# Kernel tuning notes

Hardware: AMD Instinct MI355X
Metric: run time of the kernel (lower is better)

Reference implementation:

```python
import jax, jax.numpy as jnp
import numpy as np

KSIZE = 16  # sliding window length (module ksize)


def setup_inputs() -> dict:
    key = jax.random.key(0)
    k0, k1, k2, k3, k4 = jax.random.split(key, 5)
    B, L, D, H = 16, 1024, 256, 256
    s = 1.0 / np.sqrt(H)  # torch RNN default init: U(-1/sqrt(H), 1/sqrt(H))
    x = jax.random.normal(k0, (B, L, D), dtype=jnp.float32)
    W_ih = jax.random.uniform(k1, (3 * H, D), jnp.float32, -s, s)  # [r|z|n] rows
    W_hh = jax.random.uniform(k2, (3 * H, H), jnp.float32, -s, s)
    b_ih = jax.random.uniform(k3, (3 * H,), jnp.float32, -s, s)
    b_hh = jax.random.uniform(k4, (3 * H,), jnp.float32, -s, s)
    return {"x": x, "W_ih": W_ih, "W_hh": W_hh, "b_ih": b_ih, "b_hh": b_hh}


def reference(x, W_ih, W_hh, b_ih, b_hh):
    # LocalRNN forward: for each position l, run a GRU over the window
    # x[l-K+1 : l+1] (zero left-padded) and emit the final hidden state.
    # Instead of materializing the [B, L, K, D] windowed copy (torch get_K),
    # we scan over the K window steps, slicing the padded input each step.
    B, L, D = x.shape
    H = W_hh.shape[1]
    K = KSIZE
    xpad = jnp.concatenate([jnp.zeros((B, K - 1, D), x.dtype), x], axis=1)  # [B, L+K-1, D]

    def step(h, t):
        xt = jax.lax.dynamic_slice_in_dim(xpad, t, L, axis=1)  # [B, L, D] = window step t for every position
        gi = jnp.einsum('bld,gd->blg', xt, W_ih) + b_ih          # [B, L, 3H]
        gh = jnp.einsum('blh,gh->blg', h, W_hh) + b_hh           # [B, L, 3H]
        i_r, i_z, i_n = jnp.split(gi, 3, axis=-1)
        h_r, h_z, h_n = jnp.split(gh, 3, axis=-1)
        r = jax.nn.sigmoid(i_r + h_r)
        z = jax.nn.sigmoid(i_z + h_z)
        n = jnp.tanh(i_n + r * h_n)
        h_new = (1.0 - z) * n + z * h  # torch GRU update
        return h_new, None

    h0 = jnp.zeros((B, L, H), x.dtype)
    h_final, _ = jax.lax.scan(step, h0, jnp.arange(K))
    return h_final  # [B, L, H] == h.view(batch, l, output_dim)
```

## Files before the change

### kernel.cpp

```cpp
#include <hip/hip_runtime.h>
#include <hip/hip_bf16.h>
#include <cstdint>


#define B_  16
#define L_  1024
#define D_  256
#define H_  256
#define K_  16
#define MT  32
#define NROW 47
#define HS  264
#define GRS 258
#define GNS 264
#define L2E 1.44269504f

typedef __attribute__((ext_vector_type(8))) short  bf16x8;
typedef __attribute__((ext_vector_type(4))) float  floatx4;
typedef unsigned short ush;

#if __has_builtin(__builtin_amdgcn_exp2f)
#define fexp2(x) __builtin_amdgcn_exp2f(x)
#else
#define fexp2(x) exp2f(x)
#endif

__device__ __forceinline__ float bf2f(ush u) {
    union { unsigned int i; float f; } v; v.i = ((unsigned int)u) << 16; return v.f;
}
__device__ __forceinline__ ush f2bf(float f) {
    union { float f; unsigned int i; } v; v.f = f;
    unsigned int x = v.i;
    return (ush)((x + 0x7FFFu + ((x >> 16) & 1u)) >> 16);
}
__device__ __forceinline__ unsigned int pk2(float a, float b) {
    union { __hip_bfloat162 v; unsigned int u; } c;
    c.v = __float22bfloat162_rn(make_float2(a, b));
    return c.u;
}
__device__ __forceinline__ float rcpf(float x) { return __builtin_amdgcn_rcpf(x); }

#define NWR 196608
__global__ __launch_bounds__(256) void wprep(const float* __restrict__ Wih,
                                             const float* __restrict__ Whh,
                                             ush* __restrict__ Wir,
                                             ush* __restrict__ Wr) {
    int idx = blockIdx.x * 256 + threadIdx.x;
    const float* src = (idx < NWR) ? Whh : Wih;
    ush* dst         = (idx < NWR) ? Wr  : Wir;
    int e = (idx < NWR) ? idx : idx - NWR;
    int w    = e / 24576, r1 = e % 24576;
    int n    = r1 / 4096,  r2 = r1 % 4096;
    int ks   = r2 / 512,   r3 = r2 % 512;
    int lane = r3 >> 3,    j  = r3 & 7;
    int l16 = lane & 15, quad = lane >> 4;
    int gate = n >> 1, sloc = n & 1;
    int srow = gate * 256 + (2 * w + sloc) * 16 + l16;
    int scol = ks * 32 + quad * 8 + j;
    float scl = (gate < 2) ? -L2E : 2.f * L2E;
    dst[e] = f2bf(src[srow * 256 + scol] * scl);
}

__global__ __launch_bounds__(512, 2) void rnn_fused(const float* __restrict__ x,
                                                    const ush* __restrict__ Wir,
                                                    const ush* __restrict__ Wr,
                                                    const float* __restrict__ bih,
                                                    const float* __restrict__ bhh,
                                                    float* __restrict__ out) {
    __shared__ __align__(16) ush xs[48 * HS];
    __shared__ unsigned int grz[NROW * GRS];
    __shared__ __align__(16) ush gn[NROW * GNS];
    __shared__ __align__(16) ush hl[2][MT * HS];

    int tid  = threadIdx.x;
    int wave = tid >> 6, lane = tid & 63;
    int l16  = lane & 15, quad = lane >> 4, quad4 = quad * 4;
    int p0   = blockIdx.x * MT;
    int bb   = p0 >> 10, lb = p0 & 1023;
    int base = wave * 32 + l16;

    {
        const float4* x4 = (const float4*)x;
        for (int idx = tid; idx < 48 * 64; idx += 512) {
            int j = idx >> 6, c = idx & 63;
            int tok = lb - 15 + j;
            float4 v = make_float4(0.f, 0.f, 0.f, 0.f);
            if (tok >= 0 && tok < L_) v = x4[(size_t)((bb << 10) + tok) * 64 + c];
            *(uint2*)(xs + j * HS + c * 4) = make_uint2(pk2(v.x, v.y), pk2(v.z, v.w));
        }
        for (int idx = tid; idx < MT * HS / 2; idx += 512)
            ((unsigned int*)(&hl[0][0]))[idx] = 0u;
    }
    __syncthreads();

    {
        floatx4 gacc[3][6];
#pragma unroll
        for (int sl = 0; sl < 2; sl++) {
            int cs = base + sl * 16;
            float ir = -L2E * (bih[cs] + bhh[cs]);
            float iz = -L2E * (bih[256 + cs] + bhh[256 + cs]);
            float in_ = 2.f * L2E * bih[512 + cs];
#pragma unroll
            for (int mt = 0; mt < 3; mt++) {
                gacc[mt][0 + sl] = (floatx4){ir, ir, ir, ir};
                gacc[mt][2 + sl] = (floatx4){iz, iz, iz, iz};
                gacc[mt][4 + sl] = (floatx4){in_, in_, in_, in_};
            }
        }
        const ush* wp = Wir + (size_t)wave * 24576 + lane * 8;
#pragma unroll
        for (int ks = 0; ks < 8; ks++) {
            bf16x8 bw[6];
#pragma unroll
            for (int n = 0; n < 6; n++)
                bw[n] = *(const bf16x8*)(wp + ((n * 8 + ks) << 9));
#pragma unroll
            for (int mt = 0; mt < 3; mt++) {
                bf16x8 af = *(const bf16x8*)(xs + (mt * 16 + l16) * HS + ks * 32 + quad * 8);
#pragma unroll
                for (int n = 0; n < 6; n++)
                    gacc[mt][n] = __builtin_amdgcn_mfma_f32_16x16x32_bf16(
                        af, bw[n], gacc[mt][n], 0, 0, 0);
            }
        }
#pragma unroll
        for (int mt = 0; mt < 3; mt++)
#pragma unroll
            for (int sl = 0; sl < 2; sl++) {
                int cs = base + sl * 16;
#pragma unroll
                for (int r = 0; r < 4; r++) {
                    int j = mt * 16 + quad4 + r;
                    if (j < NROW) {
                        grz[j * GRS + cs] = pk2(gacc[mt][0 + sl][r], gacc[mt][2 + sl][r]);
                        gn[j * GNS + cs]  = f2bf(gacc[mt][4 + sl][r]);
                    }
                }
            }
    }

    bf16x8 wf[6][8];
    {
        const ush* wp = Wr + (size_t)wave * 24576 + lane * 8;
#pragma unroll
        for (int n = 0; n < 6; n++)
#pragma unroll
            for (int ks = 0; ks < 8; ks++)
                wf[n][ks] = *(const bf16x8*)(wp + ((n * 8 + ks) << 9));
    }
    float bn0 = 2.f * L2E * bhh[512 + base];
    float bn1 = 2.f * L2E * bhh[512 + base + 16];
    float hreg[16];
#pragma unroll
    for (int q = 0; q < 16; q++) hreg[q] = 0.f;
    __syncthreads();

    for (int t = 0; t < K_; t++) {
        const ush* hc  = &hl[t & 1][0];
        ush*       hnx = &hl[(t + 1) & 1][0];
#pragma unroll
        for (int T = 0; T < 2; T++) {
#pragma unroll
            for (int sl = 0; sl < 2; sl++) {
                int col = base + sl * 16;
                int r0  = T * 16 + quad4 + t;
                unsigned int c0 = grz[(r0 + 0) * GRS + col];
                unsigned int c1 = grz[(r0 + 1) * GRS + col];
                unsigned int c2 = grz[(r0 + 2) * GRS + col];
                unsigned int c3 = grz[(r0 + 3) * GRS + col];
                float bn = sl ? bn1 : bn0;
                floatx4 a0 = (floatx4){0.f, 0.f, 0.f, 0.f};
                floatx4 a1 = (floatx4){0.f, 0.f, 0.f, 0.f};
                floatx4 a2 = (floatx4){bn, bn, bn, bn};
                const ush* ha = hc + (T * 16 + l16) * HS + quad * 8;
#pragma unroll
                for (int ks = 0; ks < 8; ks++) {
                    bf16x8 af = *(const bf16x8*)(ha + ks * 32);
                    a0 = __builtin_amdgcn_mfma_f32_16x16x32_bf16(af, wf[0 + sl][ks], a0, 0, 0, 0);
                    a1 = __builtin_amdgcn_mfma_f32_16x16x32_bf16(af, wf[2 + sl][ks], a1, 0, 0, 0);
                    a2 = __builtin_amdgcn_mfma_f32_16x16x32_bf16(af, wf[4 + sl][ks], a2, 0, 0, 0);
                }
                unsigned int cc[4] = {c0, c1, c2, c3};
                int hb = (T * 16 + quad4) * HS + col;
#pragma unroll
                for (int r = 0; r < 4; r++) {
                    float ar = a0[r] + __uint_as_float(cc[r] << 16);
                    float az = a1[r] + __uint_as_float(cc[r] & 0xffff0000u);
                    float rg = rcpf(1.f + fexp2(ar));
                    float zg = rcpf(1.f + fexp2(az));
                    float u  = bf2f(gn[(r0 + r) * GNS + col]) + rg * a2[r];
                    float ng = 1.f - 2.f * rcpf(fexp2(u) + 1.f);
                    int q = T * 8 + sl * 4 + r;
                    float hv = ng + zg * (hreg[q] - ng);
                    hreg[q] = hv;
                    hnx[hb + r * HS] = f2bf(hv);
                }
            }
        }
        __syncthreads();
    }
#pragma unroll
    for (int T = 0; T < 2; T++)
#pragma unroll
        for (int sl = 0; sl < 2; sl++)
#pragma unroll
            for (int r = 0; r < 4; r++) {
                int row = T * 16 + quad4 + r, col = base + sl * 16;
                out[(size_t)(p0 + row) * H_ + col] = hreg[T * 8 + sl * 4 + r];
            }
}

extern "C" void kernel_launch(void* const* d_in, const int* in_sizes, int n_in,
                              void* d_out, int out_size, void* d_ws, size_t ws_size,
                              hipStream_t stream) {
    const float* x    = (const float*)d_in[0];
    const float* W_ih = (const float*)d_in[1];
    const float* W_hh = (const float*)d_in[2];
    const float* b_ih = (const float*)d_in[3];
    const float* b_hh = (const float*)d_in[4];
    float* out = (float*)d_out;

    char* ws = (char*)d_ws;
    ush* Wir = (ush*)ws;
    ush* Wr  = (ush*)(ws + 393216);

    wprep<<<2 * NWR / 256, 256, 0, stream>>>(W_ih, W_hh, Wir, Wr);
    rnn_fused<<<B_ * L_ / MT, 512, 0, stream>>>(x, Wir, Wr, b_ih, b_hh, out);
}
```

Before: 190.2 us.

## Split GRU work across 16 waves per block, one column slice per wave

Each block now runs 1024 threads (16 waves) instead of 512, and each wave owns one 16-column slice instead of two. The weight fragments held in registers are halved so more waves can be resident. The x window is no longer staged in LDS; it is loaded from global and packed to bf16 directly into MFMA operands. The previous hidden state is read back from LDS in bf16 rather than kept in fp32 registers, which lowers register pressure but rounds the carried state to bf16 every step. The final output is likewise read from the bf16 LDS buffer.

Result: slower. 282.7 us (+48.6%).

```diff
diff --git a/kernel.cpp b/kernel.cpp
--- a/kernel.cpp
+++ b/kernel.cpp
@@ -14,6 +14,7 @@
 #define GRS 258
 #define GNS 264
 #define L2E 1.44269504f
+#define NWR 196608
 
 typedef __attribute__((ext_vector_type(8))) short  bf16x8;
 typedef __attribute__((ext_vector_type(4))) float  floatx4;
@@ -40,7 +41,6 @@
 }
 __device__ __forceinline__ float rcpf(float x) { return __builtin_amdgcn_rcpf(x); }
 
-#define NWR 196608
 __global__ __launch_bounds__(256) void wprep(const float* __restrict__ Wih,
                                              const float* __restrict__ Whh,
                                              ush* __restrict__ Wir,
@@ -49,25 +49,23 @@
     const float* src = (idx < NWR) ? Whh : Wih;
     ush* dst         = (idx < NWR) ? Wr  : Wir;
     int e = (idx < NWR) ? idx : idx - NWR;
-    int w    = e / 24576, r1 = e % 24576;
-    int n    = r1 / 4096,  r2 = r1 % 4096;
-    int ks   = r2 / 512,   r3 = r2 % 512;
-    int lane = r3 >> 3,    j  = r3 & 7;
+    int w  = e / 12288, r1 = e % 12288;
+    int f  = r1 / 512,  r3 = r1 % 512;
+    int g  = f >> 3,    ks = f & 7;
+    int lane = r3 >> 3, j  = r3 & 7;
     int l16 = lane & 15, quad = lane >> 4;
-    int gate = n >> 1, sloc = n & 1;
-    int srow = gate * 256 + (2 * w + sloc) * 16 + l16;
+    int srow = g * 256 + w * 16 + l16;
     int scol = ks * 32 + quad * 8 + j;
-    float scl = (gate < 2) ? -L2E : 2.f * L2E;
+    float scl = (g < 2) ? -L2E : 2.f * L2E;
     dst[e] = f2bf(src[srow * 256 + scol] * scl);
 }
 
-__global__ __launch_bounds__(512, 2) void rnn_fused(const float* __restrict__ x,
-                                                    const ush* __restrict__ Wir,
-                                                    const ush* __restrict__ Wr,
-                                                    const float* __restrict__ bih,
-                                                    const float* __restrict__ bhh,
-                                                    float* __restrict__ out) {
-    __shared__ __align__(16) ush xs[48 * HS];
+__global__ __launch_bounds__(1024) void rnn_fused(const float* __restrict__ x,
+                                                  const ush* __restrict__ Wir,
+                                                  const ush* __restrict__ Wr,
+                                                  const float* __restrict__ bih,
+                                                  const float* __restrict__ bhh,
+                                                  float* __restrict__ out) {
     __shared__ unsigned int grz[NROW * GRS];
     __shared__ __align__(16) ush gn[NROW * GNS];
     __shared__ __align__(16) ush hl[2][MT * HS];
@@ -77,125 +75,105 @@
     int l16  = lane & 15, quad = lane >> 4, quad4 = quad * 4;
     int p0   = blockIdx.x * MT;
     int bb   = p0 >> 10, lb = p0 & 1023;
-    int base = wave * 32 + l16;
+    int col  = wave * 16 + l16;
+
+    for (int idx = tid; idx < MT * HS / 2; idx += 1024)
+        ((unsigned int*)(&hl[0][0]))[idx] = 0u;
 
     {
-        const float4* x4 = (const float4*)x;
-        for (int idx = tid; idx < 48 * 64; idx += 512) {
-            int j = idx >> 6, c = idx & 63;
-            int tok = lb - 15 + j;
-            float4 v = make_float4(0.f, 0.f, 0.f, 0.f);
-            if (tok >= 0 && tok < L_) v = x4[(size_t)((bb << 10) + tok) * 64 + c];
-            *(uint2*)(xs + j * HS + c * 4) = make_uint2(pk2(v.x, v.y), pk2(v.z, v.w));
-        }
-        for (int idx = tid; idx < MT * HS / 2; idx += 512)
-            ((unsigned int*)(&hl[0][0]))[idx] = 0u;
+        floatx4 g0[3], g1[3], g2[3];
+        float br = -L2E * (bih[col] + bhh[col]);
+        float bz = -L2E * (bih[256 + col] + bhh[256 + col]);
+        float bn_ = 2.f * L2E * bih[512 + col];
+#pragma unroll
+        for (int mt = 0; mt < 3; mt++) {
+            g0[mt] = (floatx4){br, br, br, br};
+            g1[mt] = (floatx4){bz, bz, bz, bz};
+            g2[mt] = (floatx4){bn_, bn_, bn_, bn_};
+        }
+        const float* xrow[3];
+        bool vld[3];
+#pragma unroll
+        for (int mt = 0; mt < 3; mt++) {
+            int tok = lb - 15 + mt * 16 + l16;
+            vld[mt]  = (unsigned)tok < (unsigned)L_;
+            xrow[mt] = x + ((size_t)((bb << 10) + (vld[mt] ? tok : 0))) * D_ + quad * 8;
+        }
+        const ush* wp = Wir + (size_t)wave * 12288 + lane * 8;
+#pragma unroll
+        for (int ks = 0; ks < 8; ks++) {
+            bf16x8 bw0 = *(const bf16x8*)(wp + ((0 * 8 + ks) << 9));
+            bf16x8 bw1 = *(const bf16x8*)(wp + ((1 * 8 + ks) << 9));
+            bf16x8 bw2 = *(const bf16x8*)(wp + ((2 * 8 + ks) << 9));
+#pragma unroll
+            for (int mt = 0; mt < 3; mt++) {
+                union { uint4 u; bf16x8 v; } af;
+                if (vld[mt]) {
+                    float4 a0 = *(const float4*)(xrow[mt] + ks * 32);
+                    float4 a1 = *(const float4*)(xrow[mt] + ks * 32 + 4);
+                    af.u = make_uint4(pk2(a0.x, a0.y), pk2(a0.z, a0.w),
+                                      pk2(a1.x, a1.y), pk2(a1.z, a1.w));
+                } else {
+                    af.u = make_uint4(0u, 0u, 0u, 0u);
+                }
+                g0[mt] = __builtin_amdgcn_mfma_f32_16x16x32_bf16(af.v, bw0, g0[mt], 0, 0, 0);
+                g1[mt] = __builtin_amdgcn_mfma_f32_16x16x32_bf16(af.v, bw1, g1[mt], 0, 0, 0);
+                g2[mt] = __builtin_amdgcn_mfma_f32_16x16x32_bf16(af.v, bw2, g2[mt], 0, 0, 0);
+            }
+        }
+#pragma unroll
+        for (int mt = 0; mt < 3; mt++)
+#pragma unroll
+            for (int r = 0; r < 4; r++) {
+                int j = mt * 16 + quad4 + r;
+                if (j < NROW) {
+                    grz[j * GRS + col] = pk2(g0[mt][r], g1[mt][r]);
+                    gn[j * GNS + col]  = f2bf(g2[mt][r]);
+                }
+            }
     }
+
+    bf16x8 wf[3][8];
+    {
+        const ush* wp = Wr + (size_t)wave * 12288 + lane * 8;
+#pragma unroll
+        for (int g = 0; g < 3; g++)
+#pragma unroll
+            for (int ks = 0; ks < 8; ks++)
+                wf[g][ks] = *(const bf16x8*)(wp + ((g * 8 + ks) << 9));
+    }
+    float bn = 2.f * L2E * bhh[512 + col];
     __syncthreads();
 
-    {
-        floatx4 gacc[3][6];
-#pragma unroll
-        for (int sl = 0; sl < 2; sl++) {
-            int cs = base + sl * 16;
-            float ir = -L2E * (bih[cs] + bhh[cs]);
-            float iz = -L2E * (bih[256 + cs] + bhh[256 + cs]);
-            float in_ = 2.f * L2E * bih[512 + cs];
-#pragma unroll
-            for (int mt = 0; mt < 3; mt++) {
-                gacc[mt][0 + sl] = (floatx4){ir, ir, ir, ir};
-                gacc[mt][2 + sl] = (floatx4){iz, iz, iz, iz};
-                gacc[mt][4 + sl] = (floatx4){in_, in_, in_, in_};
-            }
-        }
-        const ush* wp = Wir + (size_t)wave * 24576 + lane * 8;
-#pragma unroll
-        for (int ks = 0; ks < 8; ks++) {
-            bf16x8 bw[6];
-#pragma unroll
-            for (int n = 0; n < 6; n++)
-                bw[n] = *(const bf16x8*)(wp + ((n * 8 + ks) << 9));
-#pragma unroll
-            for (int mt = 0; mt < 3; mt++) {
-                bf16x8 af = *(const bf16x8*)(xs + (mt * 16 + l16) * HS + ks * 32 + quad * 8);
-#pragma unroll
-                for (int n = 0; n < 6; n++)
-                    gacc[mt][n] = __builtin_amdgcn_mfma_f32_16x16x32_bf16(
-                        af, bw[n], gacc[mt][n], 0, 0, 0);
-            }
-        }
-#pragma unroll
-        for (int mt = 0; mt < 3; mt++)
-#pragma unroll
-            for (int sl = 0; sl < 2; sl++) {
-                int cs = base + sl * 16;
-#pragma unroll
-                for (int r = 0; r < 4; r++) {
-                    int j = mt * 16 + quad4 + r;
-                    if (j < NROW) {
-                        grz[j * GRS + cs] = pk2(gacc[mt][0 + sl][r], gacc[mt][2 + sl][r]);
-                        gn[j * GNS + cs]  = f2bf(gacc[mt][4 + sl][r]);
-                    }
-                }
-            }
-    }
-
-    bf16x8 wf[6][8];
-    {
-        const ush* wp = Wr + (size_t)wave * 24576 + lane * 8;
-#pragma unroll
-        for (int n = 0; n < 6; n++)
-#pragma unroll
-            for (int ks = 0; ks < 8; ks++)
-                wf[n][ks] = *(const bf16x8*)(wp + ((n * 8 + ks) << 9));
-    }
-    float bn0 = 2.f * L2E * bhh[512 + base];
-    float bn1 = 2.f * L2E * bhh[512 + base + 16];
-    float hreg[16];
-#pragma unroll
-    for (int q = 0; q < 16; q++) hreg[q] = 0.f;
-    __syncthreads();
-
     for (int t = 0; t < K_; t++) {
-        const ush* hc  = &hl[t & 1][0];
-        ush*       hnx = &hl[(t + 1) & 1][0];
+        const ush* hc = &hl[t & 1][0];
+        ush*       hx = &hl[(t + 1) & 1][0];
 #pragma unroll
         for (int T = 0; T < 2; T++) {
-#pragma unroll
-            for (int sl = 0; sl < 2; sl++) {
-                int col = base + sl * 16;
-                int r0  = T * 16 + quad4 + t;
-                unsigned int c0 = grz[(r0 + 0) * GRS + col];
-                unsigned int c1 = grz[(r0 + 1) * GRS + col];
-                unsigned int c2 = grz[(r0 + 2) * GRS + col];
-                unsigned int c3 = grz[(r0 + 3) * GRS + col];
-                float bn = sl ? bn1 : bn0;
-                floatx4 a0 = (floatx4){0.f, 0.f, 0.f, 0.f};
-                floatx4 a1 = (floatx4){0.f, 0.f, 0.f, 0.f};
-                floatx4 a2 = (floatx4){bn, bn, bn, bn};
-                const ush* ha = hc + (T * 16 + l16) * HS + quad * 8;
-#pragma unroll
-                for (int ks = 0; ks < 8; ks++) {
-                    bf16x8 af = *(const bf16x8*)(ha + ks * 32);
-                    a0 = __builtin_amdgcn_mfma_f32_16x16x32_bf16(af, wf[0 + sl][ks], a0, 0, 0, 0);
-                    a1 = __builtin_amdgcn_mfma_f32_16x16x32_bf16(af, wf[2 + sl][ks], a1, 0, 0, 0);
-                    a2 = __builtin_amdgcn_mfma_f32_16x16x32_bf16(af, wf[4 + sl][ks], a2, 0, 0, 0);
-                }
-                unsigned int cc[4] = {c0, c1, c2, c3};
-                int hb = (T * 16 + quad4) * HS + col;
-#pragma unroll
-                for (int r = 0; r < 4; r++) {
-                    float ar = a0[r] + __uint_as_float(cc[r] << 16);
-                    float az = a1[r] + __uint_as_float(cc[r] & 0xffff0000u);
-                    float rg = rcpf(1.f + fexp2(ar));
-                    float zg = rcpf(1.f + fexp2(az));
-                    float u  = bf2f(gn[(r0 + r) * GNS + col]) + rg * a2[r];
-                    float ng = 1.f - 2.f * rcpf(fexp2(u) + 1.f);
-                    int q = T * 8 + sl * 4 + r;
-                    float hv = ng + zg * (hreg[q] - ng);
-                    hreg[q] = hv;
-                    hnx[hb + r * HS] = f2bf(hv);
-                }
+            floatx4 a0 = (floatx4){0.f, 0.f, 0.f, 0.f};
+            floatx4 a1 = (floatx4){0.f, 0.f, 0.f, 0.f};
+            floatx4 a2 = (floatx4){bn, bn, bn, bn};
+            const ush* ha = hc + (T * 16 + l16) * HS + quad * 8;
+#pragma unroll
+            for (int ks = 0; ks < 8; ks++) {
+                bf16x8 af = *(const bf16x8*)(ha + ks * 32);
+                a0 = __builtin_amdgcn_mfma_f32_16x16x32_bf16(af, wf[0][ks], a0, 0, 0, 0);
+                a1 = __builtin_amdgcn_mfma_f32_16x16x32_bf16(af, wf[1][ks], a1, 0, 0, 0);
+                a2 = __builtin_amdgcn_mfma_f32_16x16x32_bf16(af, wf[2][ks], a2, 0, 0, 0);
+            }
+#pragma unroll
+            for (int r = 0; r < 4; r++) {
+                int row = T * 16 + quad4 + r;
+                unsigned int c = grz[(row + t) * GRS + col];
+                float gv = bf2f(gn[(row + t) * GNS + col]);
+                float ar = a0[r] + __uint_as_float(c << 16);
+                float az = a1[r] + __uint_as_float(c & 0xffff0000u);
+                float rg = rcpf(1.f + fexp2(ar));
+                float zg = rcpf(1.f + fexp2(az));
+                float u  = gv + rg * a2[r];
+                float ng = 1.f - 2.f * rcpf(fexp2(u) + 1.f);
+                float ho = bf2f(hc[row * HS + col]);
+                hx[row * HS + col] = f2bf(ng + zg * (ho - ng));
             }
         }
         __syncthreads();
@@ -203,12 +181,10 @@
 #pragma unroll
     for (int T = 0; T < 2; T++)
 #pragma unroll
-        for (int sl = 0; sl < 2; sl++)
-#pragma unroll
-            for (int r = 0; r < 4; r++) {
-                int row = T * 16 + quad4 + r, col = base + sl * 16;
-                out[(size_t)(p0 + row) * H_ + col] = hreg[T * 8 + sl * 4 + r];
-            }
+        for (int r = 0; r < 4; r++) {
+            int row = T * 16 + quad4 + r;
+            out[(size_t)(p0 + row) * H_ + col] = bf2f(hl[0][row * HS + col]);
+        }
 }
 
 extern "C" void kernel_launch(void* const* d_in, const int* in_sizes, int n_in,
@@ -226,5 +202,5 @@
     ush* Wr  = (ush*)(ws + 393216);
 
     wprep<<<2 * NWR / 256, 256, 0, stream>>>(W_ih, W_hh, Wir, Wr);
-    rnn_fused<<<B_ * L_ / MT, 512, 0, stream>>>(x, Wir, Wr, b_ih, b_hh, out);
-}
+    rnn_fused<<<B_ * L_ / MT, 1024, 0, stream>>>(x, Wir, Wr, b_ih, b_hh, out);
+}
```

## Software-pipeline recurrent MFMA and gate math with double-banked accumulators

Applied to the files above, without the earlier changes.

Restructures each recurrent step so the MFMA block for one sub-tile is issued before the gate nonlinearities of the previous sub-tile. Two accumulator banks are used so matrix-core work and transcendental VALU work can overlap. The fp32 hidden-state registers are removed; the previous h is read back from the bf16 LDS buffer, which frees registers but keeps the carried state in bf16 only. Half the waves process sub-tiles in a different order, which is meant to spread LDS bank pressure. The final output is also read from bf16 LDS, so the result loses some precision.

Result: slower. 615.3 us (+223.5%).

```diff
diff --git a/kernel.cpp b/kernel.cpp
--- a/kernel.cpp
+++ b/kernel.cpp
@@ -1,6 +1,7 @@
 #include <hip/hip_runtime.h>
 #include <hip/hip_bf16.h>
 #include <cstdint>
+#include <type_traits>
 
 
 #define B_  16
@@ -14,6 +15,7 @@
 #define GRS 258
 #define GNS 264
 #define L2E 1.44269504f
+#define NWR 196608
 
 typedef __attribute__((ext_vector_type(8))) short  bf16x8;
 typedef __attribute__((ext_vector_type(4))) float  floatx4;
@@ -40,7 +42,8 @@
 }
 __device__ __forceinline__ float rcpf(float x) { return __builtin_amdgcn_rcpf(x); }
 
-#define NWR 196608
+template <int N> using ic = std::integral_constant<int, N>;
+
 __global__ __launch_bounds__(256) void wprep(const float* __restrict__ Wih,
                                              const float* __restrict__ Whh,
                                              ush* __restrict__ Wir,
@@ -151,55 +154,74 @@
     }
     float bn0 = 2.f * L2E * bhh[512 + base];
     float bn1 = 2.f * L2E * bhh[512 + base + 16];
-    float hreg[16];
-#pragma unroll
-    for (int q = 0; q < 16; q++) hreg[q] = 0.f;
     __syncthreads();
 
     for (int t = 0; t < K_; t++) {
-        const ush* hc  = &hl[t & 1][0];
-        ush*       hnx = &hl[(t + 1) & 1][0];
-#pragma unroll
-        for (int T = 0; T < 2; T++) {
-#pragma unroll
-            for (int sl = 0; sl < 2; sl++) {
-                int col = base + sl * 16;
-                int r0  = T * 16 + quad4 + t;
-                unsigned int c0 = grz[(r0 + 0) * GRS + col];
-                unsigned int c1 = grz[(r0 + 1) * GRS + col];
-                unsigned int c2 = grz[(r0 + 2) * GRS + col];
-                unsigned int c3 = grz[(r0 + 3) * GRS + col];
-                float bn = sl ? bn1 : bn0;
-                floatx4 a0 = (floatx4){0.f, 0.f, 0.f, 0.f};
-                floatx4 a1 = (floatx4){0.f, 0.f, 0.f, 0.f};
-                floatx4 a2 = (floatx4){bn, bn, bn, bn};
-                const ush* ha = hc + (T * 16 + l16) * HS + quad * 8;
-#pragma unroll
-                for (int ks = 0; ks < 8; ks++) {
-                    bf16x8 af = *(const bf16x8*)(ha + ks * 32);
-                    a0 = __builtin_amdgcn_mfma_f32_16x16x32_bf16(af, wf[0 + sl][ks], a0, 0, 0, 0);
-                    a1 = __builtin_amdgcn_mfma_f32_16x16x32_bf16(af, wf[2 + sl][ks], a1, 0, 0, 0);
-                    a2 = __builtin_amdgcn_mfma_f32_16x16x32_bf16(af, wf[4 + sl][ks], a2, 0, 0, 0);
-                }
-                unsigned int cc[4] = {c0, c1, c2, c3};
-                int hb = (T * 16 + quad4) * HS + col;
-#pragma unroll
-                for (int r = 0; r < 4; r++) {
-                    float ar = a0[r] + __uint_as_float(cc[r] << 16);
-                    float az = a1[r] + __uint_as_float(cc[r] & 0xffff0000u);
-                    float rg = rcpf(1.f + fexp2(ar));
-                    float zg = rcpf(1.f + fexp2(az));
-                    float u  = bf2f(gn[(r0 + r) * GNS + col]) + rg * a2[r];
-                    float ng = 1.f - 2.f * rcpf(fexp2(u) + 1.f);
-                    int q = T * 8 + sl * 4 + r;
-                    float hv = ng + zg * (hreg[q] - ng);
-                    hreg[q] = hv;
-                    hnx[hb + r * HS] = f2bf(hv);
-                }
-            }
-        }
+        const ush* hc = &hl[t & 1][0];
+        ush*       hx = &hl[(t + 1) & 1][0];
+
+        floatx4      A[2][3];
+        unsigned int C[2][4];
+
+        auto mfma_sub = [&](auto subc, auto bankc) {
+            constexpr int sub = decltype(subc)::value;
+            constexpr int bk  = decltype(bankc)::value;
+            constexpr int T = sub >> 1, sl = sub & 1;
+            int colx = base + sl * 16;
+            int r0 = T * 16 + quad4 + t;
+            C[bk][0] = grz[(r0 + 0) * GRS + colx];
+            C[bk][1] = grz[(r0 + 1) * GRS + colx];
+            C[bk][2] = grz[(r0 + 2) * GRS + colx];
+            C[bk][3] = grz[(r0 + 3) * GRS + colx];
+            float bnv = sl ? bn1 : bn0;
+            A[bk][0] = (floatx4){0.f, 0.f, 0.f, 0.f};
+            A[bk][1] = (floatx4){0.f, 0.f, 0.f, 0.f};
+            A[bk][2] = (floatx4){bnv, bnv, bnv, bnv};
+            const ush* ha = hc + (T * 16 + l16) * HS + quad * 8;
+#pragma unroll
+            for (int ks = 0; ks < 8; ks++) {
+                bf16x8 af = *(const bf16x8*)(ha + ks * 32);
+                A[bk][0] = __builtin_amdgcn_mfma_f32_16x16x32_bf16(af, wf[0 + sl][ks], A[bk][0], 0, 0, 0);
+                A[bk][1] = __builtin_amdgcn_mfma_f32_16x16x32_bf16(af, wf[2 + sl][ks], A[bk][1], 0, 0, 0);
+                A[bk][2] = __builtin_amdgcn_mfma_f32_16x16x32_bf16(af, wf[4 + sl][ks], A[bk][2], 0, 0, 0);
+            }
+        };
+        auto gates_sub = [&](auto subc, auto bankc) {
+            constexpr int sub = decltype(subc)::value;
+            constexpr int bk  = decltype(bankc)::value;
+            constexpr int T = sub >> 1, sl = sub & 1;
+            int colx = base + sl * 16;
+            int r0 = T * 16 + quad4 + t;
+            int hb = (T * 16 + quad4) * HS + colx;
+#pragma unroll
+            for (int r = 0; r < 4; r++) {
+                unsigned int c = C[bk][r];
+                float gv = bf2f(gn[(r0 + r) * GNS + colx]);
+                float ar = A[bk][0][r] + __uint_as_float(c << 16);
+                float az = A[bk][1][r] + __uint_as_float(c & 0xffff0000u);
+                float rg = rcpf(1.f + fexp2(ar));
+                float zg = rcpf(1.f + fexp2(az));
+                float u  = gv + rg * A[bk][2][r];
+                float ng = 1.f - 2.f * rcpf(fexp2(u) + 1.f);
+                float ho = bf2f(hc[hb + r * HS]);
+                hx[hb + r * HS] = f2bf(ng + zg * (ho - ng));
+            }
+        };
+        auto run4 = [&](auto sa, auto sb, auto sc, auto sd) {
+            mfma_sub(sa, ic<0>{});
+            mfma_sub(sb, ic<1>{});
+            gates_sub(sa, ic<0>{});
+            mfma_sub(sc, ic<0>{});
+            gates_sub(sb, ic<1>{});
+            mfma_sub(sd, ic<1>{});
+            gates_sub(sc, ic<0>{});
+            gates_sub(sd, ic<1>{});
+        };
+        if (wave & 4) run4(ic<2>{}, ic<3>{}, ic<0>{}, ic<1>{});
+        else          run4(ic<0>{}, ic<1>{}, ic<2>{}, ic<3>{});
         __syncthreads();
     }
+
 #pragma unroll
     for (int T = 0; T < 2; T++)
 #pragma unroll
@@ -207,7 +229,7 @@
 #pragma unroll
             for (int r = 0; r < 4; r++) {
                 int row = T * 16 + quad4 + r, col = base + sl * 16;
-                out[(size_t)(p0 + row) * H_ + col] = hreg[T * 8 + sl * 4 + r];
+                out[(size_t)(p0 + row) * H_ + col] = bf2f(hl[0][row * HS + col]);
             }
 }
 
```
